# Kernel optimization log

Hardware: AMD Instinct MI355X
Metric: run time of the kernel (lower is better)

## Reference

```python
import jax, jax.numpy as jnp
import numpy as np

CH = 64
GROUPS = 32
EPS = 1e-5


def setup_inputs() -> dict:
    key = jax.random.key(0)
    ks = jax.random.split(key, 10)
    b, c, h, w = 4, CH, 64, 64
    x = jax.random.normal(ks[0], (b, c, h, w), dtype=jnp.float32)
    s = 1.0 / np.sqrt(c)
    Wq = jax.random.normal(ks[1], (c, c), dtype=jnp.float32) * s
    bq = jnp.zeros((c,), dtype=jnp.float32)
    Wk = jax.random.normal(ks[2], (c, c), dtype=jnp.float32) * s
    bk = jnp.zeros((c,), dtype=jnp.float32)
    Wv = jax.random.normal(ks[3], (c, c), dtype=jnp.float32) * s
    bv = jnp.zeros((c,), dtype=jnp.float32)
    Wo = jax.random.normal(ks[4], (c, c), dtype=jnp.float32) * s
    bo = jnp.zeros((c,), dtype=jnp.float32)
    gamma = jnp.ones((c,), dtype=jnp.float32)
    beta = jnp.zeros((c,), dtype=jnp.float32)
    return {"x": x, "Wq": Wq, "bq": bq, "Wk": Wk, "bk": bk,
            "Wv": Wv, "bv": bv, "Wo": Wo, "bo": bo,
            "gamma": gamma, "beta": beta}


def group_norm(x, gamma, beta):
    b, c, h, w = x.shape
    xg = x.reshape(b, GROUPS, c // GROUPS, h, w)
    mean = jnp.mean(xg, axis=(2, 3, 4), keepdims=True)
    var = jnp.var(xg, axis=(2, 3, 4), keepdims=True)
    xn = ((xg - mean) * jax.lax.rsqrt(var + EPS)).reshape(b, c, h, w)
    return xn * gamma[None, :, None, None] + beta[None, :, None, None]


def conv1x1(x, W, bias):
    # 1x1 conv == channel matmul: x [b,c,h,w], W [out,in]
    return jnp.einsum('bchw,oc->bohw', x, W) + bias[None, :, None, None]


def reference(x, Wq, bq, Wk, bk, Wv, bv, Wo, bo, gamma, beta):
    b, c, h, w = x.shape
    n = h * w
    xn = group_norm(x, gamma, beta)
    q = conv1x1(xn, Wq, bq).reshape(b, c, n)  # [b,c,n]
    k = conv1x1(xn, Wk, bk).reshape(b, c, n)
    v = conv1x1(xn, Wv, bv).reshape(b, c, n)
    scale = 1.0 / jnp.sqrt(jnp.asarray(c, dtype=x.dtype))
    # scores: q^T k -> [b, n_q, n_k]
    attn = jax.nn.softmax(jnp.einsum('bci,bcj->bij', q, k) * scale, axis=-1)
    # out = v @ attn^T -> [b, c, n_q]
    out = jnp.einsum('bcj,bij->bci', v, attn).reshape(b, c, h, w)
    return x + conv1x1(out, Wo, bo)
```

## Files before the change

### kernel.cpp

```cpp
#include <hip/hip_runtime.h>
#include <hip/hip_bf16.h>

#define NPOS 4096
#define KS 72
#define QSCALE 0.18033688011112042f

typedef __attribute__((ext_vector_type(4))) float f32x4;
typedef __attribute__((ext_vector_type(16))) float f32x16;
typedef __attribute__((ext_vector_type(8))) short bf16x8;
typedef __attribute__((ext_vector_type(2))) int i32x2;
typedef __attribute__((ext_vector_type(2))) int iv2;

__device__ __forceinline__ short f2bf(float f) {
  union { __hip_bfloat16 h; short s; } u;
  u.h = __float2bfloat16(f);
  return u.s;
}
__device__ __forceinline__ float bf2f(short s) {
  union { float f; unsigned u; } u;
  u.u = ((unsigned)(unsigned short)s) << 16;
  return u.f;
}
__device__ __forceinline__ int pack_bf16(float lo, float hi) {
  unsigned a = (unsigned short)f2bf(lo);
  unsigned b = (unsigned short)f2bf(hi);
  return (int)(a | (b << 16));
}
__device__ __forceinline__ bf16x8 cvt8(const float* p) {
  f32x4 u = *(const f32x4*)p;
  f32x4 v = *(const f32x4*)(p + 4);
  bf16x8 r;
  r[0] = f2bf(u.x); r[1] = f2bf(u.y); r[2] = f2bf(u.z); r[3] = f2bf(u.w);
  r[4] = f2bf(v.x); r[5] = f2bf(v.y); r[6] = f2bf(v.z); r[7] = f2bf(v.w);
  return r;
}
__device__ __forceinline__ float exp2_hw(float x) { return __builtin_amdgcn_exp2f(x); }

typedef const __attribute__((address_space(1))) void* gas_ptr;
typedef __attribute__((address_space(3))) void* las_ptr;
__device__ __forceinline__ void gload_lds16(const void* g, void* l) {
  __builtin_amdgcn_global_load_lds((gas_ptr)g, (las_ptr)l, 16, 0, 0);
}

__global__ __launch_bounds__(256) void stats_kernel(const float* __restrict__ x,
                                                    float* __restrict__ stats) {
  const int bg = blockIdx.x;
  const f32x4* base = (const f32x4*)(x + (size_t)bg * 8192);
  float s = 0.f, ss = 0.f;
  for (int i = threadIdx.x; i < 2048; i += 256) {
    f32x4 v = base[i];
    s  += v.x + v.y + v.z + v.w;
    ss += v.x * v.x + v.y * v.y + v.z * v.z + v.w * v.w;
  }
  for (int off = 32; off; off >>= 1) {
    s  += __shfl_down(s, off, 64);
    ss += __shfl_down(ss, off, 64);
  }
  __shared__ float red[8];
  const int wave = threadIdx.x >> 6, lane = threadIdx.x & 63;
  if (lane == 0) { red[wave] = s; red[4 + wave] = ss; }
  __syncthreads();
  if (threadIdx.x == 0) {
    float S  = red[0] + red[1] + red[2] + red[3];
    float SS = red[4] + red[5] + red[6] + red[7];
    float mean = S * (1.f / 8192.f);
    float var  = SS * (1.f / 8192.f) - mean * mean;
    stats[2 * bg]     = mean;
    stats[2 * bg + 1] = rsqrtf(var + 1e-5f);
  }
}

__global__ __launch_bounds__(256) void qkv_kernel(
    const float* __restrict__ x,
    const float* __restrict__ Wq, const float* __restrict__ bq,
    const float* __restrict__ Wk, const float* __restrict__ bk,
    const float* __restrict__ Wv, const float* __restrict__ bv,
    const float* __restrict__ gamma, const float* __restrict__ beta,
    const float* __restrict__ stats,
    short* __restrict__ qT, short* __restrict__ kT, short* __restrict__ vC) {
  __shared__ short xn_lds[32 * KS];
  __shared__ short out_lds[32 * 200];

  const int tid  = threadIdx.x;
  const int b    = blockIdx.x >> 7;
  const int pt   = blockIdx.x & 127;
  const int p0   = pt << 5;
  const int wave = tid >> 6;
  const int lane = tid & 63;
  const int quad = lane >> 4;
  const int l16  = lane & 15;

  bf16x8 a_lo[3], a_hi[3];
  float bias_r[3][4];
  {
    const float* Wsrc[3] = {Wq, Wk, Wv};
    const float* Bsrc[3] = {bq, bk, bv};
#pragma unroll
    for (int t = 0; t < 3; t++) {
      const float* wr = Wsrc[t] + (size_t)(wave * 16 + l16) * 64;
      a_lo[t] = cvt8(wr + quad * 8);
      a_hi[t] = cvt8(wr + 32 + quad * 8);
#pragma unroll
      for (int r = 0; r < 4; r++) bias_r[t][r] = Bsrc[t][wave * 16 + quad * 4 + r];
    }
  }

  {
    const int ch = tid >> 2, pg = tid & 3;
    float mean = stats[b * 64 + 2 * (ch >> 1)];
    float rstd = stats[b * 64 + 2 * (ch >> 1) + 1];
    float sc = rstd * gamma[ch];
    float sh = beta[ch] - mean * sc;
    const float* src = x + ((size_t)(b * 64 + ch)) * NPOS + p0 + pg * 8;
    f32x4 v0 = *(const f32x4*)src;
    f32x4 v1 = *(const f32x4*)(src + 4);
    short* d = xn_lds + ch;
    d[(pg * 8 + 0) * KS] = f2bf(fmaf(v0.x, sc, sh));
    d[(pg * 8 + 1) * KS] = f2bf(fmaf(v0.y, sc, sh));
    d[(pg * 8 + 2) * KS] = f2bf(fmaf(v0.z, sc, sh));
    d[(pg * 8 + 3) * KS] = f2bf(fmaf(v0.w, sc, sh));
    d[(pg * 8 + 4) * KS] = f2bf(fmaf(v1.x, sc, sh));
    d[(pg * 8 + 5) * KS] = f2bf(fmaf(v1.y, sc, sh));
    d[(pg * 8 + 6) * KS] = f2bf(fmaf(v1.z, sc, sh));
    d[(pg * 8 + 7) * KS] = f2bf(fmaf(v1.w, sc, sh));
  }
  __syncthreads();

  const f32x4 zero4 = {0.f, 0.f, 0.f, 0.f};
#pragma unroll
  for (int n = 0; n < 2; n++) {
    const short* xr = xn_lds + (n * 16 + l16) * KS;
    bf16x8 b_lo = *(const bf16x8*)(xr + quad * 8);
    bf16x8 b_hi = *(const bf16x8*)(xr + 32 + quad * 8);
#pragma unroll
    for (int t = 0; t < 3; t++) {
      f32x4 c = zero4;
      c = __builtin_amdgcn_mfma_f32_16x16x32_bf16(a_lo[t], b_lo, c, 0, 0, 0);
      c = __builtin_amdgcn_mfma_f32_16x16x32_bf16(a_hi[t], b_hi, c, 0, 0, 0);
      float o0 = c[0] + bias_r[t][0], o1 = c[1] + bias_r[t][1];
      float o2 = c[2] + bias_r[t][2], o3 = c[3] + bias_r[t][3];
      if (t == 0) { o0 *= QSCALE; o1 *= QSCALE; o2 *= QSCALE; o3 *= QSCALE; }
      i32x2 val;
      val.x = pack_bf16(o0, o1);
      val.y = pack_bf16(o2, o3);
      *(i32x2*)(out_lds + (n * 16 + l16) * 200 + t * 64 + wave * 16 + quad * 4) = val;
    }
  }
  __syncthreads();

  {
    const int p = tid >> 3, c8 = (tid & 7) << 3;
    short* qd = qT + ((size_t)(b * NPOS + p0 + p)) * 64 + c8;
    *(bf16x8*)qd = *(const bf16x8*)(out_lds + p * 200 + c8);
    short* kd = kT + ((size_t)(b * NPOS + p0 + p)) * 64 + c8;
    *(bf16x8*)kd = *(const bf16x8*)(out_lds + p * 200 + 64 + c8);
  }
  {
    const int ch = tid >> 2, pg = tid & 3;
    bf16x8 v;
#pragma unroll
    for (int i = 0; i < 8; i++) v[i] = out_lds[(pg * 8 + i) * 200 + 128 + ch];
    *(bf16x8*)(vC + ((size_t)(b * 64 + ch)) * NPOS + p0 + pg * 8) = v;
  }
}

__global__ __launch_bounds__(256, 4) void flash6_kernel(
    const short* __restrict__ qT, const short* __restrict__ kT,
    const short* __restrict__ vC, short* __restrict__ part,
    float* __restrict__ lsum) {
  __shared__ short Kbuf[2][64 * 64];
  __shared__ short Vbuf[2][64 * 64];

  const int raw = blockIdx.x;
  const int bid = ((raw & 7) << 7) + (raw >> 3);
  const int qt    = bid & 31;
  const int chunk = (bid >> 5) & 7;
  const int b     = bid >> 8;
  const int tid   = threadIdx.x;
  const int wave  = tid >> 6;
  const int lane  = tid & 63;
  const int hi    = lane >> 5;
  const int l32   = lane & 31;
  const int m0w   = (qt << 7) + (wave << 5);
  const int jbase = chunk << 9;

  bf16x8 bq[4];
  {
    const short* qp = qT + ((size_t)(b * NPOS + m0w + l32)) * 64 + hi * 8;
#pragma unroll
    for (int cs = 0; cs < 4; cs++) bq[cs] = *(const bf16x8*)(qp + cs * 16);
  }

  f32x16 oa0, oa1;
#pragma unroll
  for (int r = 0; r < 16; r++) { oa0[r] = 0.f; oa1[r] = 0.f; }
  float lacc = 0.f;

  auto stage = [&](int bb, int kt2) {
    const int j0s = jbase + (kt2 << 6);
#pragma unroll
    for (int k = 0; k < 2; k++) {
      const int u   = k * 256 + (wave << 6) + lane;
      const int row = u >> 3;
      const int ss  = (u & 7) ^ (row & 7);
      const short* gk = kT + ((size_t)(b * NPOS + j0s + row)) * 64 + ss * 8;
      gload_lds16(gk, &Kbuf[bb][(k * 256 + (wave << 6)) * 8]);
      const short* gv = vC + ((size_t)(b * 64 + row)) * NPOS + j0s + ss * 8;
      gload_lds16(gv, &Vbuf[bb][(k * 256 + (wave << 6)) * 8]);
    }
  };

  stage(0, 0);
  int cur = 0;

#pragma unroll 2
  for (int kt = 0; kt < 8; kt++) {
    if (kt < 7) {
      stage(cur ^ 1, kt + 1);
      asm volatile("s_waitcnt vmcnt(4)" ::: "memory");
    } else {
      asm volatile("s_waitcnt vmcnt(0)" ::: "memory");
    }
    __builtin_amdgcn_sched_barrier(0);
    __builtin_amdgcn_s_barrier();
    __builtin_amdgcn_sched_barrier(0);

#pragma unroll
    for (int jt = 0; jt < 2; jt++) {
      __builtin_amdgcn_s_setprio(1);
      f32x16 s;
#pragma unroll
      for (int r = 0; r < 16; r++) s[r] = 0.f;
      const int krow = (jt << 5) + l32;
      const short* kr = &Kbuf[cur][krow * 64];
#pragma unroll
      for (int cs = 0; cs < 4; cs++) {
        bf16x8 ka = *(const bf16x8*)(kr + (((cs << 1) + hi) ^ (krow & 7)) * 8);
        s = __builtin_amdgcn_mfma_f32_32x32x16_bf16(ka, bq[cs], s, 0, 0, 0);
      }

      float p[16];
#pragma unroll
      for (int r = 0; r < 16; r++) { p[r] = exp2_hw(s[r]); lacc += p[r]; }

#pragma unroll
      for (int ks = 0; ks < 2; ks++) {
        int a0 = pack_bf16(p[ks * 8 + 0], p[ks * 8 + 1]);
        int b0 = pack_bf16(p[ks * 8 + 4], p[ks * 8 + 5]);
        int a1 = pack_bf16(p[ks * 8 + 2], p[ks * 8 + 3]);
        int b1 = pack_bf16(p[ks * 8 + 6], p[ks * 8 + 7]);
        iv2 r02 = __builtin_amdgcn_permlane32_swap(a0, b0, false, false);
        iv2 r13 = __builtin_amdgcn_permlane32_swap(a1, b1, false, false);
        union { bf16x8 v; int w[4]; } pu;
        pu.w[0] = r02[0]; pu.w[1] = r13[0]; pu.w[2] = r02[1]; pu.w[3] = r13[1];
        const bf16x8 pa = pu.v;

        const int vs = (jt << 2) + (ks << 1) + hi;
        {
          const int vrow = l32;
          bf16x8 vb = *(const bf16x8*)(&Vbuf[cur][vrow * 64] + ((vs ^ (vrow & 7)) << 3));
          oa0 = __builtin_amdgcn_mfma_f32_32x32x16_bf16(pa, vb, oa0, 0, 0, 0);
        }
        {
          const int vrow = 32 + l32;
          bf16x8 vb = *(const bf16x8*)(&Vbuf[cur][vrow * 64] + ((vs ^ (vrow & 7)) << 3));
          oa1 = __builtin_amdgcn_mfma_f32_32x32x16_bf16(pa, vb, oa1, 0, 0, 0);
        }
      }
      __builtin_amdgcn_s_setprio(0);
    }

    asm volatile("s_waitcnt lgkmcnt(0)" ::: "memory");
    __builtin_amdgcn_sched_barrier(0);
    __builtin_amdgcn_s_barrier();
    cur ^= 1;
  }

  lacc += __shfl_xor(lacc, 32, 64);
  short* pb = part + ((size_t)(b * 8 + chunk) << 18);
#pragma unroll
  for (int r = 0; r < 16; r++) {
    const int m = m0w + (r & 3) + ((r >> 2) << 3) + (hi << 2);
    pb[(size_t)m * 64 + l32]      = f2bf(oa0[r]);
    pb[(size_t)m * 64 + 32 + l32] = f2bf(oa1[r]);
  }
  if (lane < 32) lsum[((size_t)(b * 8 + chunk) << 12) + m0w + l32] = lacc;
}

__global__ __launch_bounds__(256) void co_kernel(
    const short* __restrict__ part, const float* __restrict__ lsum,
    const float* __restrict__ Wo, const float* __restrict__ bo,
    const float* __restrict__ x, float* __restrict__ y) {
  __shared__ float inv[32];
  __shared__ short attn_lds[32 * KS];
  __shared__ float y_lds[64 * 36];

  const int tid   = threadIdx.x;
  const int b     = blockIdx.x >> 7;
  const int pt    = blockIdx.x & 127;
  const int p0    = pt << 5;
  const int wave  = tid >> 6;
  const int lane  = tid & 63;
  const int quad  = lane >> 4;
  const int l16   = lane & 15;

  const float* wr = Wo + (size_t)(wave * 16 + l16) * 64;
  bf16x8 a_lo = cvt8(wr + quad * 8);
  bf16x8 a_hi = cvt8(wr + 32 + quad * 8);

  if (tid < 32) {
    float lt = 0.f;
#pragma unroll
    for (int c = 0; c < 8; c++) lt += lsum[((size_t)(b * 8 + c) << 12) + p0 + tid];
    inv[tid] = 1.f / lt;
  }
  __syncthreads();

  {
    const int r = tid >> 3, c8 = (tid & 7) << 3;
    float acc[8];
#pragma unroll
    for (int i = 0; i < 8; i++) acc[i] = 0.f;
#pragma unroll
    for (int c = 0; c < 8; c++) {
      const short* src = part + ((size_t)(b * 8 + c) << 18) + (size_t)(p0 + r) * 64 + c8;
      bf16x8 v = *(const bf16x8*)src;
#pragma unroll
      for (int i = 0; i < 8; i++) acc[i] += bf2f(v[i]);
    }
    const float iv = inv[r];
#pragma unroll
    for (int i = 0; i < 8; i++) attn_lds[r * KS + c8 + i] = f2bf(acc[i] * iv);
  }
  __syncthreads();

  const f32x4 zero4 = {0.f, 0.f, 0.f, 0.f};
#pragma unroll
  for (int n = 0; n < 2; n++) {
    const short* ar = attn_lds + (n * 16 + l16) * KS;
    bf16x8 b_lo = *(const bf16x8*)(ar + quad * 8);
    bf16x8 b_hi = *(const bf16x8*)(ar + 32 + quad * 8);
    f32x4 c = zero4;
    c = __builtin_amdgcn_mfma_f32_16x16x32_bf16(a_lo, b_lo, c, 0, 0, 0);
    c = __builtin_amdgcn_mfma_f32_16x16x32_bf16(a_hi, b_hi, c, 0, 0, 0);
#pragma unroll
    for (int r = 0; r < 4; r++)
      y_lds[(wave * 16 + quad * 4 + r) * 36 + n * 16 + l16] = c[r];
  }
  __syncthreads();

  {
    const int ch = tid >> 2, pg = tid & 3;
    const size_t off = ((size_t)(b * 64 + ch)) * NPOS + p0 + pg * 8;
    const float* xs = x + off;
    float* dst = y + off;
    float bb = bo[ch];
    const float* ys = y_lds + ch * 36 + pg * 8;
    f32x4 x0 = *(const f32x4*)xs, x1 = *(const f32x4*)(xs + 4);
    f32x4 y0 = *(const f32x4*)ys, y1 = *(const f32x4*)(ys + 4);
    f32x4 o0 = {x0.x + bb + y0.x, x0.y + bb + y0.y, x0.z + bb + y0.z, x0.w + bb + y0.w};
    f32x4 o1 = {x1.x + bb + y1.x, x1.y + bb + y1.y, x1.z + bb + y1.z, x1.w + bb + y1.w};
    *(f32x4*)dst = o0;
    *(f32x4*)(dst + 4) = o1;
  }
}

extern "C" void kernel_launch(void* const* d_in, const int* in_sizes, int n_in,
                              void* d_out, int out_size, void* d_ws, size_t ws_size,
                              hipStream_t stream) {
  const float* x     = (const float*)d_in[0];
  const float* Wq    = (const float*)d_in[1];
  const float* bq    = (const float*)d_in[2];
  const float* Wk    = (const float*)d_in[3];
  const float* bk    = (const float*)d_in[4];
  const float* Wv    = (const float*)d_in[5];
  const float* bv    = (const float*)d_in[6];
  const float* Wo    = (const float*)d_in[7];
  const float* bo    = (const float*)d_in[8];
  const float* gamma = (const float*)d_in[9];
  const float* beta  = (const float*)d_in[10];
  float* y = (float*)d_out;

  char* ws = (char*)d_ws;
  float* stats = (float*)ws;
  short* qT   = (short*)(ws + 1024);
  short* kT   = (short*)(ws + 1024 + (1u << 21));
  short* vC   = (short*)(ws + 1024 + (2u << 21));
  short* part = (short*)(ws + 1024 + (3u << 21));
  float* lsum = (float*)(ws + 1024 + (11u << 21));

  stats_kernel<<<dim3(128), dim3(256), 0, stream>>>(x, stats);
  qkv_kernel<<<dim3(512), dim3(256), 0, stream>>>(x, Wq, bq, Wk, bk, Wv, bv,
                                                  gamma, beta, stats, qT, kT, vC);
  flash6_kernel<<<dim3(1024), dim3(256), 0, stream>>>(qT, kT, vC, part, lsum);
  co_kernel<<<dim3(512), dim3(256), 0, stream>>>(part, lsum, Wo, bo, x, y);
}
```

Before: 114.5 us.

## Process two query subtiles per wave to reuse K/V LDS fragments

Each wave now handles 64 query rows (two 32-row subtiles) instead of 32, so every K and V fragment read from LDS feeds two MFMA chains. The grid is halved to 512 blocks and the block-to-work mapping is adjusted to match. This cuts LDS reads and global K/V staging per unit of work. In exchange it roughly doubles accumulator register use, drops the occupancy hint from launch bounds, and leaves fewer blocks to fill the device.

```diff
diff --git a/kernel.cpp b/kernel.cpp
--- a/kernel.cpp
+++ b/kernel.cpp
@@ -164,7 +164,7 @@
   }
 }
 
-__global__ __launch_bounds__(256, 4) void flash6_kernel(
+__global__ __launch_bounds__(256) void flash7_kernel(
     const short* __restrict__ qT, const short* __restrict__ kT,
     const short* __restrict__ vC, short* __restrict__ part,
     float* __restrict__ lsum) {
@@ -172,29 +172,34 @@
   __shared__ short Vbuf[2][64 * 64];
 
   const int raw = blockIdx.x;
-  const int bid = ((raw & 7) << 7) + (raw >> 3);
-  const int qt    = bid & 31;
-  const int chunk = (bid >> 5) & 7;
-  const int b     = bid >> 8;
+  const int bid = ((raw & 7) << 6) + (raw >> 3);
+  const int qt    = bid & 15;
+  const int chunk = (bid >> 4) & 7;
+  const int b     = bid >> 7;
   const int tid   = threadIdx.x;
   const int wave  = tid >> 6;
   const int lane  = tid & 63;
   const int hi    = lane >> 5;
   const int l32   = lane & 31;
-  const int m0w   = (qt << 7) + (wave << 5);
+  const int m0w   = (qt << 8) + (wave << 6);
   const int jbase = chunk << 9;
 
-  bf16x8 bq[4];
-  {
-    const short* qp = qT + ((size_t)(b * NPOS + m0w + l32)) * 64 + hi * 8;
-#pragma unroll
-    for (int cs = 0; cs < 4; cs++) bq[cs] = *(const bf16x8*)(qp + cs * 16);
-  }
-
-  f32x16 oa0, oa1;
-#pragma unroll
-  for (int r = 0; r < 16; r++) { oa0[r] = 0.f; oa1[r] = 0.f; }
-  float lacc = 0.f;
+  bf16x8 bq[2][4];
+#pragma unroll
+  for (int s = 0; s < 2; s++) {
+    const short* qp = qT + ((size_t)(b * NPOS + m0w + s * 32 + l32)) * 64 + hi * 8;
+#pragma unroll
+    for (int cs = 0; cs < 4; cs++) bq[s][cs] = *(const bf16x8*)(qp + cs * 16);
+  }
+
+  f32x16 oa[2][2];
+#pragma unroll
+  for (int s = 0; s < 2; s++)
+#pragma unroll
+    for (int h = 0; h < 2; h++)
+#pragma unroll
+      for (int r = 0; r < 16; r++) oa[s][h][r] = 0.f;
+  float lacc[2] = {0.f, 0.f};
 
   auto stage = [&](int bb, int kt2) {
     const int j0s = jbase + (kt2 << 6);
@@ -228,43 +233,51 @@
 #pragma unroll
     for (int jt = 0; jt < 2; jt++) {
       __builtin_amdgcn_s_setprio(1);
-      f32x16 s;
-#pragma unroll
-      for (int r = 0; r < 16; r++) s[r] = 0.f;
       const int krow = (jt << 5) + l32;
       const short* kr = &Kbuf[cur][krow * 64];
-#pragma unroll
-      for (int cs = 0; cs < 4; cs++) {
-        bf16x8 ka = *(const bf16x8*)(kr + (((cs << 1) + hi) ^ (krow & 7)) * 8);
-        s = __builtin_amdgcn_mfma_f32_32x32x16_bf16(ka, bq[cs], s, 0, 0, 0);
+      bf16x8 ka[4];
+#pragma unroll
+      for (int cs = 0; cs < 4; cs++)
+        ka[cs] = *(const bf16x8*)(kr + (((cs << 1) + hi) ^ (krow & 7)) * 8);
+
+      bf16x8 pa[2][2];
+#pragma unroll
+      for (int s = 0; s < 2; s++) {
+        f32x16 sc;
+#pragma unroll
+        for (int r = 0; r < 16; r++) sc[r] = 0.f;
+#pragma unroll
+        for (int cs = 0; cs < 4; cs++)
+          sc = __builtin_amdgcn_mfma_f32_32x32x16_bf16(ka[cs], bq[s][cs], sc, 0, 0, 0);
+
+        float p[16];
+#pragma unroll
+        for (int r = 0; r < 16; r++) { p[r] = exp2_hw(sc[r]); lacc[s] += p[r]; }
+
+#pragma unroll
+        for (int ks = 0; ks < 2; ks++) {
+          int a0 = pack_bf16(p[ks * 8 + 0], p[ks * 8 + 1]);
+          int b0 = pack_bf16(p[ks * 8 + 4], p[ks * 8 + 5]);
+          int a1 = pack_bf16(p[ks * 8 + 2], p[ks * 8 + 3]);
+          int b1 = pack_bf16(p[ks * 8 + 6], p[ks * 8 + 7]);
+          iv2 r02 = __builtin_amdgcn_permlane32_swap(a0, b0, false, false);
+          iv2 r13 = __builtin_amdgcn_permlane32_swap(a1, b1, false, false);
+          union { bf16x8 v; int w[4]; } pu;
+          pu.w[0] = r02[0]; pu.w[1] = r13[0]; pu.w[2] = r02[1]; pu.w[3] = r13[1];
+          pa[s][ks] = pu.v;
+        }
       }
 
-      float p[16];
-#pragma unroll
-      for (int r = 0; r < 16; r++) { p[r] = exp2_hw(s[r]); lacc += p[r]; }
-
 #pragma unroll
       for (int ks = 0; ks < 2; ks++) {
-        int a0 = pack_bf16(p[ks * 8 + 0], p[ks * 8 + 1]);
-        int b0 = pack_bf16(p[ks * 8 + 4], p[ks * 8 + 5]);
-        int a1 = pack_bf16(p[ks * 8 + 2], p[ks * 8 + 3]);
-        int b1 = pack_bf16(p[ks * 8 + 6], p[ks * 8 + 7]);
-        iv2 r02 = __builtin_amdgcn_permlane32_swap(a0, b0, false, false);
-        iv2 r13 = __builtin_amdgcn_permlane32_swap(a1, b1, false, false);
-        union { bf16x8 v; int w[4]; } pu;
-        pu.w[0] = r02[0]; pu.w[1] = r13[0]; pu.w[2] = r02[1]; pu.w[3] = r13[1];
-        const bf16x8 pa = pu.v;
-
         const int vs = (jt << 2) + (ks << 1) + hi;
-        {
-          const int vrow = l32;
-          bf16x8 vb = *(const bf16x8*)(&Vbuf[cur][vrow * 64] + ((vs ^ (vrow & 7)) << 3));
-          oa0 = __builtin_amdgcn_mfma_f32_32x32x16_bf16(pa, vb, oa0, 0, 0, 0);
-        }
-        {
-          const int vrow = 32 + l32;
-          bf16x8 vb = *(const bf16x8*)(&Vbuf[cur][vrow * 64] + ((vs ^ (vrow & 7)) << 3));
-          oa1 = __builtin_amdgcn_mfma_f32_32x32x16_bf16(pa, vb, oa1, 0, 0, 0);
+        const int vr0 = l32, vr1 = 32 + l32;
+        bf16x8 vb0 = *(const bf16x8*)(&Vbuf[cur][vr0 * 64] + ((vs ^ (vr0 & 7)) << 3));
+        bf16x8 vb1 = *(const bf16x8*)(&Vbuf[cur][vr1 * 64] + ((vs ^ (vr1 & 7)) << 3));
+#pragma unroll
+        for (int s = 0; s < 2; s++) {
+          oa[s][0] = __builtin_amdgcn_mfma_f32_32x32x16_bf16(pa[s][ks], vb0, oa[s][0], 0, 0, 0);
+          oa[s][1] = __builtin_amdgcn_mfma_f32_32x32x16_bf16(pa[s][ks], vb1, oa[s][1], 0, 0, 0);
         }
       }
       __builtin_amdgcn_s_setprio(0);
@@ -276,15 +289,22 @@
     cur ^= 1;
   }
 
-  lacc += __shfl_xor(lacc, 32, 64);
+  lacc[0] += __shfl_xor(lacc[0], 32, 64);
+  lacc[1] += __shfl_xor(lacc[1], 32, 64);
   short* pb = part + ((size_t)(b * 8 + chunk) << 18);
 #pragma unroll
-  for (int r = 0; r < 16; r++) {
-    const int m = m0w + (r & 3) + ((r >> 2) << 3) + (hi << 2);
-    pb[(size_t)m * 64 + l32]      = f2bf(oa0[r]);
-    pb[(size_t)m * 64 + 32 + l32] = f2bf(oa1[r]);
-  }
-  if (lane < 32) lsum[((size_t)(b * 8 + chunk) << 12) + m0w + l32] = lacc;
+  for (int s = 0; s < 2; s++)
+#pragma unroll
+    for (int r = 0; r < 16; r++) {
+      const int m = m0w + (s << 5) + (r & 3) + ((r >> 2) << 3) + (hi << 2);
+      pb[(size_t)m * 64 + l32]      = f2bf(oa[s][0][r]);
+      pb[(size_t)m * 64 + 32 + l32] = f2bf(oa[s][1][r]);
+    }
+  if (lane < 32) {
+    const size_t lb = ((size_t)(b * 8 + chunk) << 12) + m0w;
+    lsum[lb + l32]      = lacc[0];
+    lsum[lb + 32 + l32] = lacc[1];
+  }
 }
 
 __global__ __launch_bounds__(256) void co_kernel(
@@ -392,6 +412,6 @@
   stats_kernel<<<dim3(128), dim3(256), 0, stream>>>(x, stats);
   qkv_kernel<<<dim3(512), dim3(256), 0, stream>>>(x, Wq, bq, Wk, bk, Wv, bv,
                                                   gamma, beta, stats, qT, kT, vC);
-  flash6_kernel<<<dim3(1024), dim3(256), 0, stream>>>(qT, kT, vC, part, lsum);
+  flash7_kernel<<<dim3(512), dim3(256), 0, stream>>>(qT, kT, vC, part, lsum);
   co_kernel<<<dim3(512), dim3(256), 0, stream>>>(part, lsum, Wo, bo, x, y);
 }
```

Result: slower. 118.0 us (+3.0%).
